# Performance work log

Measured on AMD Instinct MI355X. Metric: run time of the kernel, lower is better.

Reference implementation:

```python
import jax, jax.numpy as jnp
import numpy as np

B, N, H = 1, 4096, 2048
NH, HD = 16, H // 16
WINDOW = 4096
EPS = 1e-6
THETA = 10000.0
NEG = -1e30


def rmsnorm(x, w):
    var = jnp.mean(jnp.square(x.astype(jnp.float32)), axis=-1, keepdims=True)
    return (x * jax.lax.rsqrt(var + EPS)).astype(w.dtype) * w


def rotate_half(x):
    x1, x2 = x[..., : x.shape[-1] // 2], x[..., x.shape[-1] // 2 :]
    return jnp.concatenate((-x2, x1), axis=-1)


def setup_inputs() -> dict:
    key = jax.random.key(0)
    k1, k2, k3 = jax.random.split(key, 3)
    x = jax.random.normal(k1, (B, N, H), dtype=jnp.float32)
    w_qkv = jax.random.normal(k2, (H, 3 * H), dtype=jnp.float32) * (1.0 / np.sqrt(H))
    w_out = jax.random.normal(k3, (H, H), dtype=jnp.float32) * (1.0 / np.sqrt(H))
    q_gamma = jnp.ones((HD,), dtype=jnp.float32)
    k_gamma = jnp.ones((HD,), dtype=jnp.float32)
    return {"x": x, "w_qkv": w_qkv, "w_out": w_out, "q_gamma": q_gamma, "k_gamma": k_gamma}


def reference(x, w_qkv, w_out, q_gamma, k_gamma):
    b, n, _ = x.shape
    qkv = jnp.einsum('bnh,hm->bnm', x, w_qkv)  # [b,n,3H]
    q, k, v = jnp.split(qkv, 3, axis=-1)
    # [b, nh, n, hd]
    q = q.reshape(b, n, NH, HD).transpose(0, 2, 1, 3)
    k = k.reshape(b, n, NH, HD).transpose(0, 2, 1, 3)
    v = v.reshape(b, n, NH, HD).transpose(0, 2, 1, 3)
    # qk RMSNorm over head_dim
    q = rmsnorm(q, q_gamma)
    k = rmsnorm(k, k_gamma)
    # RoPE
    inv_freq = 1.0 / (THETA ** (jnp.arange(0, HD, 2, dtype=jnp.float32) / HD))
    t = jnp.arange(n, dtype=jnp.float32)
    freqs = t[:, None] * inv_freq[None, :]          # [n, hd/2]
    emb = jnp.concatenate((freqs, freqs), axis=-1)  # [n, hd]
    cos = jnp.cos(emb)[None, None, :, :]
    sin = jnp.sin(emb)[None, None, :, :]
    q = q * cos + rotate_half(q) * sin
    k = k * cos + rotate_half(k) * sin
    # causal + sliding-window mask (kv not truncated since n == WINDOW)
    kv_len = k.shape[-2]
    q_idx = jnp.arange(n)[:, None] + (kv_len - n)
    k_idx = jnp.arange(kv_len)[None, :]
    mask = (q_idx >= k_idx) & (q_idx - k_idx <= WINDOW)
    scores = jnp.einsum('bhqd,bhkd->bhqk', q, k) / np.sqrt(HD)
    scores = jnp.where(mask[None, None, :, :], scores, NEG)
    attn = jax.nn.softmax(scores, axis=-1)
    out = jnp.einsum('bhqk,bhkd->bhqd', attn, v)
    out = out.transpose(0, 2, 1, 3).reshape(b, n, H)
    return jnp.einsum('bnh,hm->bnm', out, w_out)
```

## Files before the change

kernel.cpp:

```cpp
#include <hip/hip_runtime.h>
#include <stdint.h>

typedef short bf16x8 __attribute__((ext_vector_type(8)));
typedef float f32x4 __attribute__((ext_vector_type(4)));
typedef unsigned short u16;

__device__ __forceinline__ float b2f(u16 u) {
  return __uint_as_float(((unsigned)u) << 16);
}
__device__ __forceinline__ u16 f2b(float f) {
  unsigned u = __float_as_uint(f);
  return (u16)((u + 0x7fffu + ((u >> 16) & 1u)) >> 16);
}

#define NEGINF (-1.0e30f)

__device__ __forceinline__ void gld_lds16(const u16* g, u16* l) {
  __builtin_amdgcn_global_load_lds(
      (const __attribute__((address_space(1))) unsigned int*)(const void*)g,
      (__attribute__((address_space(3))) unsigned int*)(void*)l, 16, 0, 0);
}

__global__ void sniff5(const u16* x, const u16* wq, const u16* wo,
                       const u16* qg, const u16* kg, int* flags) {
  const u16* p;
  int S;
  switch (blockIdx.x) {
    case 0: p = x;  S = 2048; break;
    case 1: p = wq; S = 2048; break;
    case 2: p = wo; S = 2048; break;
    case 3: p = qg; S = 128;  break;
    default: p = kg; S = 128; break;
  }
  __shared__ int cbig, czero;
  if (threadIdx.x == 0) { cbig = 0; czero = 0; }
  __syncthreads();
  int cb = 0, cz = 0;
  for (int i = threadIdx.x; i < S; i += 256) {
    const u16 u = p[i];
    if (((u >> 7) & 0xFF) >= 0xC0) ++cb;
    if (!(i & 1) && u == 0) ++cz;
  }
  atomicAdd(&cbig, cb);
  atomicAdd(&czero, cz);
  __syncthreads();
  if (threadIdx.x == 0)
    flags[blockIdx.x] = (cbig > S / 32 || czero > 3 * S / 8) ? 1 : 0;
}

__global__ __launch_bounds__(256) void conv_in(const void* __restrict__ src,
                                               u16* __restrict__ dst,
                                               const int* __restrict__ flags,
                                               int fidx, int n) {
  const int fp32 = flags[fidx];
  int i = blockIdx.x * 256 + threadIdx.x;
  const int stride = gridDim.x * 256;
  if (fp32) {
    const float* s = (const float*)src;
    for (; i < n; i += stride) dst[i] = f2b(s[i]);
  } else {
    const u16* s = (const u16*)src;
    for (; i < n; i += stride) dst[i] = s[i];
  }
}

__global__ __launch_bounds__(256) void transpose_in(
    const void* __restrict__ src, u16* __restrict__ dst,
    const int* __restrict__ flags, int fidx, int ss, int ds) {
  __shared__ u16 tile[64][65];
  const int fp32 = flags[fidx];
  const int rb = blockIdx.y * 64, cb = blockIdx.x * 64;
  const int cl = threadIdx.x & 63, r0 = threadIdx.x >> 6;
  if (fp32) {
    const float* s = (const float*)src;
#pragma unroll
    for (int i = 0; i < 16; ++i) {
      int r = r0 + i * 4;
      tile[r][cl] = f2b(s[(long long)(rb + r) * ss + cb + cl]);
    }
  } else {
    const u16* s = (const u16*)src;
#pragma unroll
    for (int i = 0; i < 16; ++i) {
      int r = r0 + i * 4;
      tile[r][cl] = s[(long long)(rb + r) * ss + cb + cl];
    }
  }
  __syncthreads();
#pragma unroll
  for (int i = 0; i < 16; ++i) {
    int r2 = r0 + i * 4;
    dst[(long long)(cb + r2) * ds + rb + cl] = tile[cl][r2];
  }
}

__global__ __launch_bounds__(256) void transpose_bf16(
    const u16* __restrict__ src, u16* __restrict__ dst, int ss, int ds,
    long long sz, long long dz) {
  __shared__ u16 tile[64][65];
  const u16* s = src + (long long)blockIdx.z * sz;
  u16* d = dst + (long long)blockIdx.z * dz;
  const int rb = blockIdx.y * 64, cb = blockIdx.x * 64;
  const int cl = threadIdx.x & 63, r0 = threadIdx.x >> 6;
#pragma unroll
  for (int i = 0; i < 16; ++i) {
    int r = r0 + i * 4;
    tile[r][cl] = s[(long long)(rb + r) * ss + cb + cl];
  }
  __syncthreads();
#pragma unroll
  for (int i = 0; i < 16; ++i) {
    int r2 = r0 + i * 4;
    d[(long long)(cb + r2) * ds + rb + cl] = tile[cl][r2];
  }
}

__global__ __launch_bounds__(256) void gemm_qkv(
    const u16* __restrict__ A, const u16* __restrict__ Bt,
    u16* __restrict__ Cq, u16* __restrict__ Ck, u16* __restrict__ Cv, int K) {
  __shared__ __align__(16) u16 As[128 * 32];
  __shared__ __align__(16) u16 Bs[128 * 32];
  const int bid = blockIdx.x;
  const int xcd = bid & 7, lid = bid >> 3;
  const int mb = lid / 6, nsub = lid - mb * 6;
  const int nb = xcd * 6 + nsub;
  const int m0 = mb * 128;
  const int n0g = nb * 128;
  const int sel = nb >> 4;
  u16* C = sel == 0 ? Cq : (sel == 1 ? Ck : Cv);
  const int n0 = (nb & 15) * 128;
  const int tid = threadIdx.x;
  const int w = tid >> 6, l = tid & 63;
  const int lane15 = l & 15, quad = l >> 4;
  const int wm = (w >> 1) * 64, wn = (w & 1) * 64;
  const int srow = w * 32 + (l >> 2);
  const int skoff = (((l & 3) ^ ((l >> 3) & 3))) * 8;
  const u16* gA = A + (size_t)(m0 + srow) * K + skoff;
  const u16* gB = Bt + (size_t)(n0g + srow) * K + skoff;
  u16* lA = &As[w * 1024];
  u16* lB = &Bs[w * 1024];
  const int rq = (quad ^ ((lane15 >> 1) & 3)) * 8;
  f32x4 acc[4][4] = {};
  const int nK = K >> 5;
  for (int kb = 0; kb < nK; ++kb) {
    __syncthreads();
    gld_lds16(gA, lA);
    gld_lds16(gA + (size_t)16 * K, lA + 512);
    gld_lds16(gB, lB);
    gld_lds16(gB + (size_t)16 * K, lB + 512);
    __syncthreads();
    bf16x8 af[4], bfr[4];
#pragma unroll
    for (int mi = 0; mi < 4; ++mi)
      af[mi] = *(const bf16x8*)&As[(wm + mi * 16 + lane15) * 32 + rq];
#pragma unroll
    for (int ni = 0; ni < 4; ++ni)
      bfr[ni] = *(const bf16x8*)&Bs[(wn + ni * 16 + lane15) * 32 + rq];
#pragma unroll
    for (int mi = 0; mi < 4; ++mi)
#pragma unroll
      for (int ni = 0; ni < 4; ++ni)
        acc[mi][ni] = __builtin_amdgcn_mfma_f32_16x16x32_bf16(
            af[mi], bfr[ni], acc[mi][ni], 0, 0, 0);
    gA += 32;
    gB += 32;
  }
#pragma unroll
  for (int mi = 0; mi < 4; ++mi)
#pragma unroll
    for (int ni = 0; ni < 4; ++ni)
#pragma unroll
      for (int r = 0; r < 4; ++r)
        C[(size_t)(m0 + wm + mi * 16 + quad * 4 + r) * 2048 +
          (n0 + wn + ni * 16 + lane15)] = f2b(acc[mi][ni][r]);
}

__global__ __launch_bounds__(256) void gemm_bt_f32(
    const u16* __restrict__ A, const u16* __restrict__ Bt,
    float* __restrict__ C, int K) {
  __shared__ __align__(16) u16 As[128 * 32];
  __shared__ __align__(16) u16 Bs[128 * 32];
  const int bid = blockIdx.x;
  const int xcd = bid & 7, lid = bid >> 3;
  const int mb = lid >> 1, nsub = lid & 1;
  const int nb = xcd * 2 + nsub;
  const int m0 = mb * 128, n0 = nb * 128;
  const int tid = threadIdx.x;
  const int w = tid >> 6, l = tid & 63;
  const int lane15 = l & 15, quad = l >> 4;
  const int wm = (w >> 1) * 64, wn = (w & 1) * 64;
  const int srow = w * 32 + (l >> 2);
  const int skoff = (((l & 3) ^ ((l >> 3) & 3))) * 8;
  const u16* gA = A + (size_t)(m0 + srow) * K + skoff;
  const u16* gB = Bt + (size_t)(n0 + srow) * K + skoff;
  u16* lA = &As[w * 1024];
  u16* lB = &Bs[w * 1024];
  const int rq = (quad ^ ((lane15 >> 1) & 3)) * 8;
  f32x4 acc[4][4] = {};
  const int nK = K >> 5;
  for (int kb = 0; kb < nK; ++kb) {
    __syncthreads();
    gld_lds16(gA, lA);
    gld_lds16(gA + (size_t)16 * K, lA + 512);
    gld_lds16(gB, lB);
    gld_lds16(gB + (size_t)16 * K, lB + 512);
    __syncthreads();
    bf16x8 af[4], bfr[4];
#pragma unroll
    for (int mi = 0; mi < 4; ++mi)
      af[mi] = *(const bf16x8*)&As[(wm + mi * 16 + lane15) * 32 + rq];
#pragma unroll
    for (int ni = 0; ni < 4; ++ni)
      bfr[ni] = *(const bf16x8*)&Bs[(wn + ni * 16 + lane15) * 32 + rq];
#pragma unroll
    for (int mi = 0; mi < 4; ++mi)
#pragma unroll
      for (int ni = 0; ni < 4; ++ni)
        acc[mi][ni] = __builtin_amdgcn_mfma_f32_16x16x32_bf16(
            af[mi], bfr[ni], acc[mi][ni], 0, 0, 0);
    gA += 32;
    gB += 32;
  }
#pragma unroll
  for (int mi = 0; mi < 4; ++mi)
#pragma unroll
    for (int ni = 0; ni < 4; ++ni)
#pragma unroll
      for (int r = 0; r < 4; ++r)
        C[(size_t)(m0 + wm + mi * 16 + quad * 4 + r) * 2048 +
          (n0 + wn + ni * 16 + lane15)] = acc[mi][ni][r];
}

__global__ __launch_bounds__(256) void rms_rope(
    const u16* __restrict__ in, const u16* __restrict__ gamma,
    u16* __restrict__ outr) {
  const int wid = blockIdx.x * 4 + (threadIdx.x >> 6);
  const int l = threadIdx.x & 63;
  const int n = wid >> 4;
  const int h = wid & 15;
  const u16* base = in + (size_t)n * 2048 + h * 128;
  float a = b2f(base[l]), b = b2f(base[l + 64]);
  float ssum = a * a + b * b;
#pragma unroll
  for (int m = 1; m < 64; m <<= 1) ssum += __shfl_xor(ssum, m);
  const float r = rsqrtf(ssum * (1.0f / 128.0f) + 1e-6f);
  a *= r * b2f(gamma[l]);
  b *= r * b2f(gamma[l + 64]);
  const float inv = __expf(-(float)l * 0.14391156831212787f);
  float s, c;
  sincosf((float)n * inv, &s, &c);
  const size_t o = ((size_t)h * 4096 + n) * 128 + l;
  outr[o] = f2b(a * c - b * s);
  outr[o + 64] = f2b(b * c + a * s);
}

__device__ __forceinline__ int swzK(int o) {
  return o ^ ((((o) >> 7) & 7) << 3);
}
__device__ __forceinline__ int swzV(int o) {
  return o ^ ((((o) >> 6) & 7) << 3);
}

__global__ __launch_bounds__(256, 2) void flash_attn(
    const u16* __restrict__ q_r, const u16* __restrict__ k_r,
    const u16* __restrict__ v_t, u16* __restrict__ attn) {
  __shared__ __align__(16) u16 Kt[64 * 128];
  __shared__ __align__(16) u16 Vt[128 * 64];
  __shared__ __align__(16) u16 Pt[128 * 64];
  const int b = blockIdx.x;
  const int h = b & 15;
  const int qt = (b < 256) ? (31 - (b >> 4)) : ((b - 256) >> 4);
  const int m0 = qt * 128;
  const int tid = threadIdx.x, w = tid >> 6, l = tid & 63;
  const int lane15 = l & 15, quad = l >> 4;

  bf16x8 aq[2][4];
#pragma unroll
  for (int mi = 0; mi < 2; ++mi)
#pragma unroll
    for (int ks = 0; ks < 4; ++ks)
      aq[mi][ks] = *(const bf16x8*)&q_r[((size_t)h * 4096 + m0 + w * 32 +
                                         mi * 16 + lane15) * 128 +
                                        ks * 32 + quad * 8];

  f32x4 acc_o[2][8] = {};
  float m_i[2][4], l_i[2][4];
#pragma unroll
  for (int mi = 0; mi < 2; ++mi)
#pragma unroll
    for (int r = 0; r < 4; ++r) {
      m_i[mi][r] = NEGINF;
      l_i[mi][r] = 0.f;
    }

  const int jend = m0 + 64;
  for (int j0 = 0; j0 <= jend; j0 += 64) {
    __syncthreads();
#pragma unroll
    for (int i = 0; i < 4; ++i) {
      const int rg = i * 4 + w;
      const int keyr = rg * 4 + (l >> 4);
      const int kc = (l & 15) ^ (keyr & 7);
      const int dr = rg * 8 + (l >> 3);
      const int vc = (l & 7) ^ (dr & 7);
      gld_lds16(&k_r[((size_t)h * 4096 + j0 + keyr) * 128 + kc * 8],
                &Kt[rg * 512]);
      gld_lds16(&v_t[((size_t)h * 128 + dr) * 4096 + j0 + vc * 8],
                &Vt[rg * 512]);
    }
    __syncthreads();

    f32x4 s2[2][4] = {};
#pragma unroll
    for (int ni = 0; ni < 4; ++ni) {
#pragma unroll
      for (int ks = 0; ks < 4; ++ks) {
        bf16x8 bk = *(const bf16x8*)&Kt[swzK((ni * 16 + lane15) * 128 +
                                             ks * 32 + quad * 8)];
        s2[0][ni] = __builtin_amdgcn_mfma_f32_16x16x32_bf16(aq[0][ks], bk,
                                                            s2[0][ni], 0, 0, 0);
        s2[1][ni] = __builtin_amdgcn_mfma_f32_16x16x32_bf16(aq[1][ks], bk,
                                                            s2[1][ni], 0, 0, 0);
      }
    }

    const float sc = 0.08838834764831845f;
    const bool mt = (j0 >= m0);
#pragma unroll
    for (int mi = 0; mi < 2; ++mi) {
#pragma unroll
      for (int r = 0; r < 4; ++r) {
        const int lrow = w * 32 + mi * 16 + quad * 4 + r;
        float xv[4], mx4 = NEGINF;
#pragma unroll
        for (int ni = 0; ni < 4; ++ni) {
          float xx = s2[mi][ni][r] * sc;
          if (mt && (j0 + ni * 16 + lane15 > m0 + lrow)) xx = NEGINF;
          xv[ni] = xx;
          mx4 = fmaxf(mx4, xx);
        }
        const float mold = m_i[mi][r];
        const unsigned long long bal = __ballot(mx4 > mold + 8.0f);
        float mcur = mold;
        if (((unsigned)(bal >> (quad * 16)) & 0xFFFFu) != 0u) {
          float mx = mx4;
#pragma unroll
          for (int mk = 1; mk < 16; mk <<= 1)
            mx = fmaxf(mx, __shfl_xor(mx, mk));
          const float mnew = fmaxf(mold, mx);
          const float alpha = __expf(mold - mnew);
          l_i[mi][r] *= alpha;
          m_i[mi][r] = mnew;
          mcur = mnew;
#pragma unroll
          for (int ni = 0; ni < 8; ++ni) acc_o[mi][ni][r] *= alpha;
        }
        float rs = 0.f;
#pragma unroll
        for (int ni = 0; ni < 4; ++ni) {
          const float p = __expf(xv[ni] - mcur);
          Pt[swzV(lrow * 64 + ni * 16 + lane15)] = f2b(p);
          rs += p;
        }
        l_i[mi][r] += rs;
      }
    }

#pragma unroll
    for (int ks = 0; ks < 2; ++ks) {
      bf16x8 ap0 = *(const bf16x8*)&Pt[swzV((w * 32 + lane15) * 64 + ks * 32 +
                                            quad * 8)];
      bf16x8 ap1 = *(const bf16x8*)&Pt[swzV((w * 32 + 16 + lane15) * 64 +
                                            ks * 32 + quad * 8)];
#pragma unroll
      for (int ni = 0; ni < 8; ++ni) {
        bf16x8 bv = *(const bf16x8*)&Vt[swzV((ni * 16 + lane15) * 64 +
                                             ks * 32 + quad * 8)];
        acc_o[0][ni] = __builtin_amdgcn_mfma_f32_16x16x32_bf16(
            ap0, bv, acc_o[0][ni], 0, 0, 0);
        acc_o[1][ni] = __builtin_amdgcn_mfma_f32_16x16x32_bf16(
            ap1, bv, acc_o[1][ni], 0, 0, 0);
      }
    }
  }

#pragma unroll
  for (int mi = 0; mi < 2; ++mi)
#pragma unroll
    for (int r = 0; r < 4; ++r) {
      float s = l_i[mi][r];
#pragma unroll
      for (int mk = 1; mk < 16; mk <<= 1) s += __shfl_xor(s, mk);
      l_i[mi][r] = s;
    }
#pragma unroll
  for (int mi = 0; mi < 2; ++mi)
#pragma unroll
    for (int ni = 0; ni < 8; ++ni)
#pragma unroll
      for (int r = 0; r < 4; ++r)
        attn[(size_t)(m0 + w * 32 + mi * 16 + quad * 4 + r) * 2048 + h * 128 +
             ni * 16 + lane15] = f2b(acc_o[mi][ni][r] / l_i[mi][r]);
}

extern "C" void kernel_launch(void* const* d_in, const int* in_sizes, int n_in,
                              void* d_out, int out_size, void* d_ws,
                              size_t ws_size, hipStream_t stream) {
  (void)out_size; (void)ws_size;
  int ix = 0, iwq = 1, iwo = 2, ig1 = 3, ig2 = 4;
  {
    int g1 = -1, g2 = -1, xx = -1, wqq = -1, woo = -1;
    for (int i = 0; i < n_in; ++i) {
      const int s = in_sizes[i];
      if (s == 8388608) xx = i;
      else if (s == 12582912) wqq = i;
      else if (s == 4194304) woo = i;
      else if (s == 128) { if (g1 < 0) g1 = i; else g2 = i; }
    }
    if (xx >= 0 && wqq >= 0 && woo >= 0 && g1 >= 0 && g2 >= 0) {
      ix = xx; iwq = wqq; iwo = woo; ig1 = g1; ig2 = g2;
    }
  }
  const void* x = d_in[ix];
  const void* wq = d_in[iwq];
  const void* wo = d_in[iwo];
  const void* qg = d_in[ig1];
  const void* kg = d_in[ig2];
  float* out = (float*)d_out;
  char* ws = (char*)d_ws;
  u16* xb = (u16*)(ws);
  u16* k_buf = (u16*)(ws + 16777216LL);
  u16* wT = (u16*)(ws + 33554432LL);
  int* flags = (int*)(ws + 58720256LL);
  u16* gq_b = (u16*)(ws + 58720512LL);
  u16* gk_b = (u16*)(ws + 58721024LL);
  u16* q_r = (u16*)(ws);
  u16* attn = (u16*)(ws + 16777216LL);
  u16* v_t = (u16*)(ws + 33554432LL);
  u16* woT = (u16*)(ws + 50331648LL);
  u16* q_buf = (u16*)d_out;
  u16* k_r = (u16*)d_out;
  u16* v_buf = (u16*)d_out + 8388608;

  sniff5<<<5, 256, 0, stream>>>((const u16*)x, (const u16*)wq, (const u16*)wo,
                                (const u16*)qg, (const u16*)kg, flags);
  conv_in<<<8192, 256, 0, stream>>>(x, xb, flags, 0, 4096 * 2048);
  conv_in<<<1, 256, 0, stream>>>(qg, gq_b, flags, 3, 128);
  conv_in<<<1, 256, 0, stream>>>(kg, gk_b, flags, 4, 128);
  transpose_in<<<dim3(96, 32), 256, 0, stream>>>(wq, wT, flags, 1, 6144, 2048);
  gemm_qkv<<<dim3(1536), 256, 0, stream>>>(xb, wT, q_buf, k_buf, v_buf, 2048);
  rms_rope<<<dim3(16384), 256, 0, stream>>>(q_buf, gq_b, q_r);
  rms_rope<<<dim3(16384), 256, 0, stream>>>(k_buf, gk_b, k_r);
  transpose_bf16<<<dim3(2, 64, 16), 256, 0, stream>>>(v_buf, v_t, 2048, 4096,
                                                      128LL, 524288LL);
  transpose_in<<<dim3(32, 32), 256, 0, stream>>>(wo, woT, flags, 2, 2048, 2048);
  flash_attn<<<dim3(512), 256, 0, stream>>>(q_r, k_r, v_t, attn);
  gemm_bt_f32<<<dim3(512), 256, 0, stream>>>(attn, woT, out, 2048);
}
```

Before: 566.6 us.

## Halve flash-attention query tile to 64 rows for more blocks and occupancy

The attention kernel now gives each block 64 query rows instead of 128, one 16-row MFMA tile per wave, and launches 1024 blocks with launch bounds raised to 4 blocks per CU. Register and LDS use per block shrink, the P tile is halved, and the causal loop ends exactly at the diagonal tile. The aim is more parallelism and occupancy to hide latency, at the cost of loading each K/V tile twice as often, since every K/V load is now shared by half as many query rows.

New measurement: 1.182 ms. 2.09x slower.

```diff
diff --git a/kernel.cpp b/kernel.cpp
--- a/kernel.cpp
+++ b/kernel.cpp
@@ -261,40 +261,36 @@
   return o ^ ((((o) >> 6) & 7) << 3);
 }
 
-__global__ __launch_bounds__(256, 2) void flash_attn(
+__global__ __launch_bounds__(256, 4) void flash_attn(
     const u16* __restrict__ q_r, const u16* __restrict__ k_r,
     const u16* __restrict__ v_t, u16* __restrict__ attn) {
   __shared__ __align__(16) u16 Kt[64 * 128];
   __shared__ __align__(16) u16 Vt[128 * 64];
-  __shared__ __align__(16) u16 Pt[128 * 64];
+  __shared__ __align__(16) u16 Pt[64 * 64];
   const int b = blockIdx.x;
   const int h = b & 15;
-  const int qt = (b < 256) ? (31 - (b >> 4)) : ((b - 256) >> 4);
-  const int m0 = qt * 128;
+  const int t = b >> 4;
+  const int qt = (b < 512) ? (63 - t) : (t - 32);
+  const int m0 = qt * 64;
   const int tid = threadIdx.x, w = tid >> 6, l = tid & 63;
   const int lane15 = l & 15, quad = l >> 4;
 
-  bf16x8 aq[2][4];
-#pragma unroll
-  for (int mi = 0; mi < 2; ++mi)
-#pragma unroll
-    for (int ks = 0; ks < 4; ++ks)
-      aq[mi][ks] = *(const bf16x8*)&q_r[((size_t)h * 4096 + m0 + w * 32 +
-                                         mi * 16 + lane15) * 128 +
-                                        ks * 32 + quad * 8];
-
-  f32x4 acc_o[2][8] = {};
-  float m_i[2][4], l_i[2][4];
-#pragma unroll
-  for (int mi = 0; mi < 2; ++mi)
-#pragma unroll
-    for (int r = 0; r < 4; ++r) {
-      m_i[mi][r] = NEGINF;
-      l_i[mi][r] = 0.f;
-    }
-
-  const int jend = m0 + 64;
-  for (int j0 = 0; j0 <= jend; j0 += 64) {
+  bf16x8 aq[4];
+#pragma unroll
+  for (int ks = 0; ks < 4; ++ks)
+    aq[ks] = *(const bf16x8*)&q_r[((size_t)h * 4096 + m0 + w * 16 + lane15) *
+                                      128 +
+                                  ks * 32 + quad * 8];
+
+  f32x4 acc_o[8] = {};
+  float m_i[4], l_i[4];
+#pragma unroll
+  for (int r = 0; r < 4; ++r) {
+    m_i[r] = NEGINF;
+    l_i[r] = 0.f;
+  }
+
+  for (int j0 = 0; j0 <= m0; j0 += 64) {
     __syncthreads();
 #pragma unroll
     for (int i = 0; i < 4; ++i) {
@@ -310,97 +306,83 @@
     }
     __syncthreads();
 
-    f32x4 s2[2][4] = {};
+    f32x4 s2[4] = {};
 #pragma unroll
     for (int ni = 0; ni < 4; ++ni) {
 #pragma unroll
       for (int ks = 0; ks < 4; ++ks) {
         bf16x8 bk = *(const bf16x8*)&Kt[swzK((ni * 16 + lane15) * 128 +
                                              ks * 32 + quad * 8)];
-        s2[0][ni] = __builtin_amdgcn_mfma_f32_16x16x32_bf16(aq[0][ks], bk,
-                                                            s2[0][ni], 0, 0, 0);
-        s2[1][ni] = __builtin_amdgcn_mfma_f32_16x16x32_bf16(aq[1][ks], bk,
-                                                            s2[1][ni], 0, 0, 0);
+        s2[ni] = __builtin_amdgcn_mfma_f32_16x16x32_bf16(aq[ks], bk, s2[ni], 0,
+                                                         0, 0);
       }
     }
 
     const float sc = 0.08838834764831845f;
     const bool mt = (j0 >= m0);
 #pragma unroll
-    for (int mi = 0; mi < 2; ++mi) {
-#pragma unroll
-      for (int r = 0; r < 4; ++r) {
-        const int lrow = w * 32 + mi * 16 + quad * 4 + r;
-        float xv[4], mx4 = NEGINF;
-#pragma unroll
-        for (int ni = 0; ni < 4; ++ni) {
-          float xx = s2[mi][ni][r] * sc;
-          if (mt && (j0 + ni * 16 + lane15 > m0 + lrow)) xx = NEGINF;
-          xv[ni] = xx;
-          mx4 = fmaxf(mx4, xx);
-        }
-        const float mold = m_i[mi][r];
-        const unsigned long long bal = __ballot(mx4 > mold + 8.0f);
-        float mcur = mold;
-        if (((unsigned)(bal >> (quad * 16)) & 0xFFFFu) != 0u) {
-          float mx = mx4;
-#pragma unroll
-          for (int mk = 1; mk < 16; mk <<= 1)
-            mx = fmaxf(mx, __shfl_xor(mx, mk));
-          const float mnew = fmaxf(mold, mx);
-          const float alpha = __expf(mold - mnew);
-          l_i[mi][r] *= alpha;
-          m_i[mi][r] = mnew;
-          mcur = mnew;
-#pragma unroll
-          for (int ni = 0; ni < 8; ++ni) acc_o[mi][ni][r] *= alpha;
-        }
-        float rs = 0.f;
-#pragma unroll
-        for (int ni = 0; ni < 4; ++ni) {
-          const float p = __expf(xv[ni] - mcur);
-          Pt[swzV(lrow * 64 + ni * 16 + lane15)] = f2b(p);
-          rs += p;
-        }
-        l_i[mi][r] += rs;
+    for (int r = 0; r < 4; ++r) {
+      const int lrow = w * 16 + quad * 4 + r;
+      float xv[4], mx4 = NEGINF;
+#pragma unroll
+      for (int ni = 0; ni < 4; ++ni) {
+        float xx = s2[ni][r] * sc;
+        if (mt && (j0 + ni * 16 + lane15 > m0 + lrow)) xx = NEGINF;
+        xv[ni] = xx;
+        mx4 = fmaxf(mx4, xx);
       }
+      const float mold = m_i[r];
+      const unsigned long long bal = __ballot(mx4 > mold + 8.0f);
+      float mcur = mold;
+      if (((unsigned)(bal >> (quad * 16)) & 0xFFFFu) != 0u) {
+        float mx = mx4;
+#pragma unroll
+        for (int mk = 1; mk < 16; mk <<= 1) mx = fmaxf(mx, __shfl_xor(mx, mk));
+        const float mnew = fmaxf(mold, mx);
+        const float alpha = __expf(mold - mnew);
+        l_i[r] *= alpha;
+        m_i[r] = mnew;
+        mcur = mnew;
+#pragma unroll
+        for (int ni = 0; ni < 8; ++ni) acc_o[ni][r] *= alpha;
+      }
+      float rs = 0.f;
+#pragma unroll
+      for (int ni = 0; ni < 4; ++ni) {
+        const float p = __expf(xv[ni] - mcur);
+        Pt[swzV(lrow * 64 + ni * 16 + lane15)] = f2b(p);
+        rs += p;
+      }
+      l_i[r] += rs;
     }
 
 #pragma unroll
     for (int ks = 0; ks < 2; ++ks) {
-      bf16x8 ap0 = *(const bf16x8*)&Pt[swzV((w * 32 + lane15) * 64 + ks * 32 +
-                                            quad * 8)];
-      bf16x8 ap1 = *(const bf16x8*)&Pt[swzV((w * 32 + 16 + lane15) * 64 +
-                                            ks * 32 + quad * 8)];
+      bf16x8 ap = *(const bf16x8*)&Pt[swzV((w * 16 + lane15) * 64 + ks * 32 +
+                                           quad * 8)];
 #pragma unroll
       for (int ni = 0; ni < 8; ++ni) {
         bf16x8 bv = *(const bf16x8*)&Vt[swzV((ni * 16 + lane15) * 64 +
                                              ks * 32 + quad * 8)];
-        acc_o[0][ni] = __builtin_amdgcn_mfma_f32_16x16x32_bf16(
-            ap0, bv, acc_o[0][ni], 0, 0, 0);
-        acc_o[1][ni] = __builtin_amdgcn_mfma_f32_16x16x32_bf16(
-            ap1, bv, acc_o[1][ni], 0, 0, 0);
+        acc_o[ni] =
+            __builtin_amdgcn_mfma_f32_16x16x32_bf16(ap, bv, acc_o[ni], 0, 0, 0);
       }
     }
   }
 
 #pragma unroll
-  for (int mi = 0; mi < 2; ++mi)
-#pragma unroll
-    for (int r = 0; r < 4; ++r) {
-      float s = l_i[mi][r];
-#pragma unroll
-      for (int mk = 1; mk < 16; mk <<= 1) s += __shfl_xor(s, mk);
-      l_i[mi][r] = s;
-    }
-#pragma unroll
-  for (int mi = 0; mi < 2; ++mi)
-#pragma unroll
-    for (int ni = 0; ni < 8; ++ni)
-#pragma unroll
-      for (int r = 0; r < 4; ++r)
-        attn[(size_t)(m0 + w * 32 + mi * 16 + quad * 4 + r) * 2048 + h * 128 +
-             ni * 16 + lane15] = f2b(acc_o[mi][ni][r] / l_i[mi][r]);
+  for (int r = 0; r < 4; ++r) {
+    float s = l_i[r];
+#pragma unroll
+    for (int mk = 1; mk < 16; mk <<= 1) s += __shfl_xor(s, mk);
+    l_i[r] = s;
+  }
+#pragma unroll
+  for (int ni = 0; ni < 8; ++ni)
+#pragma unroll
+    for (int r = 0; r < 4; ++r)
+      attn[(size_t)(m0 + w * 16 + quad * 4 + r) * 2048 + h * 128 + ni * 16 +
+           lane15] = f2b(acc_o[ni][r] / l_i[r]);
 }
 
 extern "C" void kernel_launch(void* const* d_in, const int* in_sizes, int n_in,
@@ -454,6 +436,6 @@
   transpose_bf16<<<dim3(2, 64, 16), 256, 0, stream>>>(v_buf, v_t, 2048, 4096,
                                                       128LL, 524288LL);
   transpose_in<<<dim3(32, 32), 256, 0, stream>>>(wo, woT, flags, 2, 2048, 2048);
-  flash_attn<<<dim3(512), 256, 0, stream>>>(q_r, k_r, v_t, attn);
+  flash_attn<<<dim3(1024), 256, 0, stream>>>(q_r, k_r, v_t, attn);
   gemm_bt_f32<<<dim3(512), 256, 0, stream>>>(attn, woT, out, 2048);
 }
```

## Double-buffer K/V tiles in flash attention with async prefetch

Applied to the files above, without the earlier changes.

Adds a second LDS buffer for K and V tiles. The next tile is issued via global_load_lds before computing on the current one, with explicit vmcnt waits and barriers replacing the load-then-sync pattern. This aims to hide global memory latency behind the QK and PV MFMA work. LDS usage per block rises, which could limit occupancy, and the manual waitcnt counting relies on exactly 8 outstanding loads per stage.

After: 566.5 us. About the same (-0.0%).

```diff
diff --git a/kernel.cpp b/kernel.cpp
--- a/kernel.cpp
+++ b/kernel.cpp
@@ -264,8 +264,8 @@
 __global__ __launch_bounds__(256, 2) void flash_attn(
     const u16* __restrict__ q_r, const u16* __restrict__ k_r,
     const u16* __restrict__ v_t, u16* __restrict__ attn) {
-  __shared__ __align__(16) u16 Kt[64 * 128];
-  __shared__ __align__(16) u16 Vt[128 * 64];
+  __shared__ __align__(16) u16 Kt[2][64 * 128];
+  __shared__ __align__(16) u16 Vt[2][128 * 64];
   __shared__ __align__(16) u16 Pt[128 * 64];
   const int b = blockIdx.x;
   const int h = b & 15;
@@ -293,29 +293,52 @@
       l_i[mi][r] = 0.f;
     }
 
-  const int jend = m0 + 64;
-  for (int j0 = 0; j0 <= jend; j0 += 64) {
-    __syncthreads();
+  const int keyr0 = (l >> 4);
+  const int kc = (l & 15);
+  const int dr0 = (l >> 3);
+  const int vc = (l & 7);
+
+  auto STAGE = [&](int j0, int bufi) {
 #pragma unroll
     for (int i = 0; i < 4; ++i) {
       const int rg = i * 4 + w;
-      const int keyr = rg * 4 + (l >> 4);
-      const int kc = (l & 15) ^ (keyr & 7);
-      const int dr = rg * 8 + (l >> 3);
-      const int vc = (l & 7) ^ (dr & 7);
-      gld_lds16(&k_r[((size_t)h * 4096 + j0 + keyr) * 128 + kc * 8],
-                &Kt[rg * 512]);
-      gld_lds16(&v_t[((size_t)h * 128 + dr) * 4096 + j0 + vc * 8],
-                &Vt[rg * 512]);
-    }
-    __syncthreads();
+      const int keyr = rg * 4 + keyr0;
+      const int dr = rg * 8 + dr0;
+      gld_lds16(
+          &k_r[((size_t)h * 4096 + j0 + keyr) * 128 + (kc ^ (keyr & 7)) * 8],
+          &Kt[bufi][rg * 512]);
+      gld_lds16(
+          &v_t[((size_t)h * 128 + dr) * 4096 + j0 + (vc ^ (dr & 7)) * 8],
+          &Vt[bufi][rg * 512]);
+    }
+  };
+
+  const int jend = m0 + 64;
+  STAGE(0, 0);
+  int cur = 0;
+
+  for (int j0 = 0; j0 <= jend; j0 += 64) {
+    __builtin_amdgcn_s_barrier();
+    __builtin_amdgcn_sched_barrier(0);
+    if (j0 + 64 <= jend) {
+      STAGE(j0 + 64, cur ^ 1);
+      __builtin_amdgcn_sched_barrier(0);
+      asm volatile("s_waitcnt vmcnt(8)" ::: "memory");
+    } else {
+      asm volatile("s_waitcnt vmcnt(0)" ::: "memory");
+    }
+    __builtin_amdgcn_s_barrier();
+    __builtin_amdgcn_sched_barrier(0);
+
+    const u16* Kc = Kt[cur];
+    const u16* Vc = Vt[cur];
 
     f32x4 s2[2][4] = {};
 #pragma unroll
     for (int ni = 0; ni < 4; ++ni) {
 #pragma unroll
       for (int ks = 0; ks < 4; ++ks) {
-        bf16x8 bk = *(const bf16x8*)&Kt[swzK((ni * 16 + lane15) * 128 +
+        bf16x8 bk = *(const bf16x8*)&Kc[swzK((ni * 16 + lane15) * 128 +
                                              ks * 32 + quad * 8)];
         s2[0][ni] = __builtin_amdgcn_mfma_f32_16x16x32_bf16(aq[0][ks], bk,
                                                             s2[0][ni], 0, 0, 0);
@@ -374,7 +397,7 @@
                                             ks * 32 + quad * 8)];
 #pragma unroll
       for (int ni = 0; ni < 8; ++ni) {
-        bf16x8 bv = *(const bf16x8*)&Vt[swzV((ni * 16 + lane15) * 64 +
+        bf16x8 bv = *(const bf16x8*)&Vc[swzV((ni * 16 + lane15) * 64 +
                                              ks * 32 + quad * 8)];
         acc_o[0][ni] = __builtin_amdgcn_mfma_f32_16x16x32_bf16(
             ap0, bv, acc_o[0][ni], 0, 0, 0);
@@ -382,6 +405,7 @@
             ap1, bv, acc_o[1][ni], 0, 0, 0);
       }
     }
+    cur ^= 1;
   }
 
 #pragma unroll
```
